# Optimization experiments

Measured on AMD Instinct MI355X. Metric: run time of the kernel, lower is better.

The kernel has to match this reference:

```python
import jax, jax.numpy as jnp
import numpy as np
from jax import lax

T, B, C = 50, 50, 4096
PADLEN = 49
ORDER = 2
BANDS = [(0.05, 0.15), (0.2, 0.4)]


def _butter_bandpass_sos(n, w1, w2):
    """Butterworth bandpass design (scipy.signal.iirfilter(..., ftype='butter', output='sos') equivalent)."""
    fs = 2.0
    warped = 2.0 * fs * np.tan(np.pi * np.array([w1, w2]) / fs)  # pre-warped analog freqs
    bw = warped[1] - warped[0]
    wo = np.sqrt(warped[0] * warped[1])
    k = np.arange(1, n + 1)
    p = -np.exp(1j * np.pi * (2 * k - 1) / (2 * n))  # analog LP prototype poles
    # lp2bp: n poles -> 2n poles, n zeros at origin, gain *= bw**n
    p_lp = p * bw / 2.0
    disc = np.sqrt(p_lp ** 2 - wo ** 2 + 0j)
    p_bp = np.concatenate([p_lp + disc, p_lp - disc])
    # bilinear transform (fs=2): zeros at origin -> +1; n zeros at infinity -> -1
    fs2 = 2.0 * fs
    p_d = (fs2 + p_bp) / (fs2 - p_bp)
    gain = (bw ** n) * (fs2 ** n) / np.real(np.prod(fs2 - p_bp))
    # pair conjugate poles into biquads; numerator (z-1)(z+1) = [1, 0, -1]
    pos = p_d[np.imag(p_d) > 0]
    assert len(pos) == n, 'expected complex-conjugate pole pairs'
    sos = []
    for i, pp in enumerate(pos):
        a = np.array([1.0, -2.0 * np.real(pp), np.abs(pp) ** 2])
        b = np.array([1.0, 0.0, -1.0])
        if i == 0:
            b = b * gain
        sos.append(np.concatenate([b, a]))
    return np.array(sos)  # [n_sections, 6]


def _sosfilt_zi(sos):
    """scipy.signal.sosfilt_zi: steady-state per-section initial conditions (DF2T)."""
    n_sections = sos.shape[0]
    zi = np.zeros((n_sections, 2))
    scale = 1.0
    for s in range(n_sections):
        b, a = sos[s, :3], sos[s, 3:]
        B0 = b[1] - a[1] * b[0]
        B1 = b[2] - a[2] * b[0]
        det = 1.0 + a[1] + a[2]
        zi[s, 0] = scale * (B0 + B1) / det
        zi[s, 1] = scale * ((1.0 + a[1]) * B1 - a[2] * B0) / det
        scale *= b.sum() / a.sum()
    return zi


def _sosfilt(sos, x, zi):
    """Cascaded biquads, direct form II transposed, scan over time axis 0.
    x: [T, B, C]; zi: list of (z0, z1) each [B, C]."""
    y = x
    for s in range(sos.shape[0]):
        b0, b1, b2 = (float(sos[s, 0]), float(sos[s, 1]), float(sos[s, 2]))
        a1, a2 = float(sos[s, 4]), float(sos[s, 5])
        def step(carry, xt, b0=b0, b1=b1, b2=b2, a1=a1, a2=a2):
            z0, z1 = carry
            yt = b0 * xt + z0
            return (b1 * xt + z1 - a1 * yt, b2 * xt - a2 * yt), yt
        _, y = lax.scan(step, (zi[s][0], zi[s][1]), y)
    return y


def _odd_ext(x, n):
    left = 2.0 * x[0] - x[n:0:-1]
    right = 2.0 * x[-1] - x[-2:-n - 2:-1]
    return jnp.concatenate([left, x, right], axis=0)


def _sosfiltfilt(sos, x, padlen):
    zi = _sosfilt_zi(sos)  # [S, 2] numpy
    ext = _odd_ext(x, padlen)  # [T + 2*padlen, B, C]
    x0 = ext[0]
    zi_f = [(float(zi[s, 0]) * x0, float(zi[s, 1]) * x0) for s in range(sos.shape[0])]
    y = _sosfilt(sos, ext, zi_f)
    y = y[::-1]
    y0 = y[0]
    zi_b = [(float(zi[s, 0]) * y0, float(zi[s, 1]) * y0) for s in range(sos.shape[0])]
    y = _sosfilt(sos, y, zi_b)
    y = y[::-1]
    return y[padlen:-padlen]


def _tensor_zscore(x):
    # Faithful to the original expand([50,-1,-1]).permute(1,0,2) quirk:
    # mean/std over axis 0 give [B, C]; the permute aligns them with the TIME axis,
    # i.e. out[t, b, c] = (x[t, b, c] - m[t, c]) / s[t, c]  (valid since T == B == 50).
    m = x.mean(axis=0)
    s = x.std(axis=0, ddof=1)  # torch.std default is unbiased
    return (x - m[:, None, :]) / s[:, None, :]


def setup_inputs() -> dict:
    key = jax.random.key(0)
    sample = jax.random.normal(key, (T, B, C), dtype=jnp.float32)
    return {"sample": sample}


def reference(sample):
    outs = []
    for (w1, w2) in BANDS:
        sos = _butter_bandpass_sos(ORDER, w1, w2)
        y = _sosfiltfilt(sos, sample, PADLEN)
        y = y - y.mean(axis=0)  # bandpass branch: mean-center
        y = _tensor_zscore(y)   # normalize=True
        outs.append(y)
    return jnp.stack(outs)  # [n_bands, T, B, C]
```

## Files before the change

### kernel.cpp

```cpp
#include <hip/hip_runtime.h>
#include <cmath>
#include <complex>

constexpr int TT  = 50;
constexpr int NB  = 50;
constexpr int NC  = 4096;
constexpr int NCH = NB * NC;
constexpr int PAD = 49;
constexpr int EXT = TT + 2 * PAD;
constexpr int CT  = 16;

struct Coefs {
    double b0[2][2], b1[2][2], b2[2][2], a1[2][2], a2[2][2];
    double zi0[2][2], zi1[2][2];
};

__global__ void __launch_bounds__(64) build_M(float* __restrict__ Mt, Coefs cf) {
    __shared__ double e[EXT][TT];
    const int band = blockIdx.x;
    const int j = threadIdx.x;
    if (j >= TT) return;

    const double b0a = cf.b0[band][0], b1a = cf.b1[band][0], b2a = cf.b2[band][0];
    const double a1a = cf.a1[band][0], a2a = cf.a2[band][0];
    const double b0b = cf.b0[band][1], b1b = cf.b1[band][1], b2b = cf.b2[band][1];
    const double a1b = cf.a1[band][1], a2b = cf.a2[band][1];

    const double x0 = (j == 0 ? 2.0 : 0.0) - (j == PAD ? 1.0 : 0.0);

    double za0 = cf.zi0[band][0] * x0, za1 = cf.zi1[band][0] * x0;
    double zb0 = cf.zi0[band][1] * x0, zb1 = cf.zi1[band][1] * x0;

    double ylast = 0.0;
#pragma unroll
    for (int i = 0; i < EXT; ++i) {
        double xt;
        if (i < PAD) {
            xt = (j == 0 ? 2.0 : 0.0) - (j == (PAD - i) ? 1.0 : 0.0);
        } else if (i < PAD + TT) {
            xt = (j == (i - PAD) ? 1.0 : 0.0);
        } else {
            xt = (j == TT - 1 ? 2.0 : 0.0) - (j == (2 * TT - 2 + PAD - i) ? 1.0 : 0.0);
        }
        const double y0 = b0a * xt + za0;
        za0 = b1a * xt + za1 - a1a * y0;
        za1 = b2a * xt - a2a * y0;
        const double y1 = b0b * y0 + zb0;
        zb0 = b1b * y0 + zb1 - a1b * y1;
        zb1 = b2b * y0 - a2b * y1;
        e[i][j] = y1;
        ylast = y1;
    }

    za0 = cf.zi0[band][0] * ylast; za1 = cf.zi1[band][0] * ylast;
    zb0 = cf.zi0[band][1] * ylast; zb1 = cf.zi1[band][1] * ylast;
#pragma unroll 4
    for (int m = 0; m < EXT; ++m) {
        const int i = EXT - 1 - m;
        const double xt = e[i][j];
        const double y0 = b0a * xt + za0;
        za0 = b1a * xt + za1 - a1a * y0;
        za1 = b2a * xt - a2a * y0;
        const double y1 = b0b * y0 + zb0;
        zb0 = b1b * y0 + zb1 - a1b * y1;
        zb1 = b2b * y0 - a2b * y1;
        e[i][j] = y1;
    }

    double mean = 0.0;
#pragma unroll
    for (int t = 0; t < TT; ++t) mean += e[PAD + t][j];
    mean *= (1.0 / TT);
#pragma unroll
    for (int t = 0; t < TT; ++t)
        Mt[(band * TT + j) * TT + t] = (float)(e[PAD + t][j] - mean);
}

__global__ __launch_bounds__(CT * NB) __attribute__((amdgpu_waves_per_eu(1, 4)))
void fused_bn(const float* __restrict__ x, const float* __restrict__ Mt,
              float* __restrict__ out) {
    const int tx   = threadIdx.x;
    const int b    = threadIdx.y;
    const int band = blockIdx.y;
    const int c    = blockIdx.x * CT + tx;
    const int i    = b * NC + c;

    __shared__ float sm_mu [NB][CT];
    __shared__ float sm_inv[NB][CT];

    const float* __restrict__ Mb   = Mt + band * (TT * TT);
    const float* __restrict__ xcol = x + i;

    float f[TT];
#pragma unroll
    for (int t = 0; t < TT; ++t) f[t] = 0.f;

#pragma unroll 5
    for (int k = 0; k < TT; ++k) {
        const float xk = xcol[(size_t)k * NCH];
        const float* __restrict__ r = Mb + k * TT;
#pragma unroll
        for (int t = 0; t < TT; ++t) f[t] = fmaf(r[t], xk, f[t]);
    }

    float mu = 0.f;
#pragma unroll
    for (int t = 0; t < TT; ++t) mu += f[t];
    mu *= (1.0f / TT);
    float ss = 0.f;
#pragma unroll
    for (int t = 0; t < TT; ++t) {
        const float h = f[t] - mu;
        ss = fmaf(h, h, ss);
    }
    const float inv = 1.0f / sqrtf(ss * (1.0f / (TT - 1)));

    sm_mu [b][tx] = mu;
    sm_inv[b][tx] = inv;
    __syncthreads();

    float* __restrict__ ob = out + (size_t)band * TT * NCH;
#pragma unroll
    for (int t = 0; t < TT; ++t) {
        const float v = (f[t] - sm_mu[t][tx]) * sm_inv[t][tx];
        ob[(size_t)t * NCH + i] = v;
    }
}

static Coefs make_coefs() {
    Coefs cf;
    const double bands[2][2] = {{0.05, 0.15}, {0.2, 0.4}};
    const int n = 2;
    for (int bd = 0; bd < 2; ++bd) {
        const double fs = 2.0;
        const double w1 = bands[bd][0], w2 = bands[bd][1];
        const double warped0 = 2.0 * fs * std::tan(M_PI * w1 / fs);
        const double warped1 = 2.0 * fs * std::tan(M_PI * w2 / fs);
        const double bw = warped1 - warped0;
        const double wo = std::sqrt(warped0 * warped1);
        std::complex<double> p_bp[4];
        for (int k = 1; k <= n; ++k) {
            std::complex<double> p = -std::exp(std::complex<double>(0.0, M_PI * (2 * k - 1) / (2.0 * n)));
            std::complex<double> plp = p * (bw / 2.0);
            std::complex<double> disc = std::sqrt(plp * plp - std::complex<double>(wo * wo, 0.0));
            p_bp[k - 1] = plp + disc;
            p_bp[n + k - 1] = plp - disc;
        }
        const double fs2 = 2.0 * fs;
        std::complex<double> prod(1.0, 0.0);
        for (int i = 0; i < 2 * n; ++i) prod *= (fs2 - p_bp[i]);
        const double gain = std::pow(bw, n) * std::pow(fs2, n) / prod.real();
        std::complex<double> p_d[4];
        for (int i = 0; i < 2 * n; ++i) p_d[i] = (fs2 + p_bp[i]) / (fs2 - p_bp[i]);
        double sos[2][6];
        int cnt = 0;
        for (int i = 0; i < 2 * n; ++i) {
            if (p_d[i].imag() > 0) {
                const double g = (cnt == 0) ? gain : 1.0;
                sos[cnt][0] = g;
                sos[cnt][1] = 0.0;
                sos[cnt][2] = -g;
                sos[cnt][3] = 1.0;
                sos[cnt][4] = -2.0 * p_d[i].real();
                sos[cnt][5] = std::norm(p_d[i]);
                ++cnt;
            }
        }
        double scale = 1.0;
        for (int s = 0; s < 2; ++s) {
            const double b0 = sos[s][0], b1 = sos[s][1], b2 = sos[s][2];
            const double a1 = sos[s][4], a2 = sos[s][5];
            const double B0 = b1 - a1 * b0, B1 = b2 - a2 * b0;
            const double det = 1.0 + a1 + a2;
            cf.b0[bd][s] = b0; cf.b1[bd][s] = b1; cf.b2[bd][s] = b2;
            cf.a1[bd][s] = a1; cf.a2[bd][s] = a2;
            cf.zi0[bd][s] = scale * (B0 + B1) / det;
            cf.zi1[bd][s] = scale * ((1.0 + a1) * B1 - a2 * B0) / det;
            scale *= (b0 + b1 + b2) / (1.0 + a1 + a2);
        }
    }
    return cf;
}

extern "C" void kernel_launch(void* const* d_in, const int* in_sizes, int n_in,
                              void* d_out, int out_size, void* d_ws, size_t ws_size,
                              hipStream_t stream) {
    const float* x = (const float*)d_in[0];
    float* out = (float*)d_out;
    float* Mt = (float*)d_ws;

    const Coefs cf = make_coefs();
    build_M<<<dim3(2), dim3(64), 0, stream>>>(Mt, cf);
    fused_bn<<<dim3(NC / CT, 2), dim3(CT, NB), 0, stream>>>(x, Mt, out);
}
```

Measured before the change: 153.4 us.

## Compute both filter bands per block to share input loads

Each block now applies both band matrices to the same input column, keeping two sets of 50 accumulators and writing both output bands. This halves global reads of the input and halves the grid size. In exchange it doubles per-thread register demand, which risks spilling or lower occupancy, and leaves fewer blocks for latency hiding.

```diff
diff --git a/kernel.cpp b/kernel.cpp
--- a/kernel.cpp
+++ b/kernel.cpp
@@ -79,51 +79,72 @@
 __global__ __launch_bounds__(CT * NB) __attribute__((amdgpu_waves_per_eu(1, 4)))
 void fused_bn(const float* __restrict__ x, const float* __restrict__ Mt,
               float* __restrict__ out) {
-    const int tx   = threadIdx.x;
-    const int b    = threadIdx.y;
-    const int band = blockIdx.y;
-    const int c    = blockIdx.x * CT + tx;
-    const int i    = b * NC + c;
-
-    __shared__ float sm_mu [NB][CT];
-    __shared__ float sm_inv[NB][CT];
-
-    const float* __restrict__ Mb   = Mt + band * (TT * TT);
+    const int tx = threadIdx.x;
+    const int b  = threadIdx.y;
+    const int c  = blockIdx.x * CT + tx;
+    const int i  = b * NC + c;
+
+    __shared__ float sm_mu [2][NB][CT];
+    __shared__ float sm_inv[2][NB][CT];
+
+    const float* __restrict__ M0   = Mt;
+    const float* __restrict__ M1   = Mt + TT * TT;
     const float* __restrict__ xcol = x + i;
 
-    float f[TT];
-#pragma unroll
-    for (int t = 0; t < TT; ++t) f[t] = 0.f;
+    float f0[TT], f1[TT];
+#pragma unroll
+    for (int t = 0; t < TT; ++t) { f0[t] = 0.f; f1[t] = 0.f; }
 
 #pragma unroll 5
     for (int k = 0; k < TT; ++k) {
         const float xk = xcol[(size_t)k * NCH];
-        const float* __restrict__ r = Mb + k * TT;
-#pragma unroll
-        for (int t = 0; t < TT; ++t) f[t] = fmaf(r[t], xk, f[t]);
-    }
-
-    float mu = 0.f;
-#pragma unroll
-    for (int t = 0; t < TT; ++t) mu += f[t];
-    mu *= (1.0f / TT);
-    float ss = 0.f;
+        const float* __restrict__ r0 = M0 + k * TT;
+#pragma unroll
+        for (int t = 0; t < TT; ++t) f0[t] = fmaf(r0[t], xk, f0[t]);
+        const float* __restrict__ r1 = M1 + k * TT;
+#pragma unroll
+        for (int t = 0; t < TT; ++t) f1[t] = fmaf(r1[t], xk, f1[t]);
+    }
+
+    {
+        float mu = 0.f;
+#pragma unroll
+        for (int t = 0; t < TT; ++t) mu += f0[t];
+        mu *= (1.0f / TT);
+        float ss = 0.f;
+#pragma unroll
+        for (int t = 0; t < TT; ++t) {
+            const float h = f0[t] - mu;
+            ss = fmaf(h, h, ss);
+        }
+        sm_mu [0][b][tx] = mu;
+        sm_inv[0][b][tx] = 1.0f / sqrtf(ss * (1.0f / (TT - 1)));
+    }
+    {
+        float mu = 0.f;
+#pragma unroll
+        for (int t = 0; t < TT; ++t) mu += f1[t];
+        mu *= (1.0f / TT);
+        float ss = 0.f;
+#pragma unroll
+        for (int t = 0; t < TT; ++t) {
+            const float h = f1[t] - mu;
+            ss = fmaf(h, h, ss);
+        }
+        sm_mu [1][b][tx] = mu;
+        sm_inv[1][b][tx] = 1.0f / sqrtf(ss * (1.0f / (TT - 1)));
+    }
+    __syncthreads();
+
 #pragma unroll
     for (int t = 0; t < TT; ++t) {
-        const float h = f[t] - mu;
-        ss = fmaf(h, h, ss);
-    }
-    const float inv = 1.0f / sqrtf(ss * (1.0f / (TT - 1)));
-
-    sm_mu [b][tx] = mu;
-    sm_inv[b][tx] = inv;
-    __syncthreads();
-
-    float* __restrict__ ob = out + (size_t)band * TT * NCH;
+        const float v = (f0[t] - sm_mu[0][t][tx]) * sm_inv[0][t][tx];
+        out[(size_t)t * NCH + i] = v;
+    }
 #pragma unroll
     for (int t = 0; t < TT; ++t) {
-        const float v = (f[t] - sm_mu[t][tx]) * sm_inv[t][tx];
-        ob[(size_t)t * NCH + i] = v;
+        const float v = (f1[t] - sm_mu[1][t][tx]) * sm_inv[1][t][tx];
+        out[(size_t)(TT + t) * NCH + i] = v;
     }
 }
 
@@ -191,5 +212,5 @@
 
     const Coefs cf = make_coefs();
     build_M<<<dim3(2), dim3(64), 0, stream>>>(Mt, cf);
-    fused_bn<<<dim3(NC / CT, 2), dim3(CT, NB), 0, stream>>>(x, Mt, out);
-}
+    fused_bn<<<dim3(NC / CT), dim3(CT, NB), 0, stream>>>(x, Mt, out);
+}
```

Result: slower. 199.9 us (+30.3%).
